# Kernel tuning notes

Measured on AMD Instinct MI355X. Metric: run time of the kernel, lower is better.

Reference implementation:

```python
import jax, jax.numpy as jnp
import numpy as np

N_NODES = 100000
N_EDGES = 3200000
F_IN = 512
HIDDEN = 16
N_CLASS = 10


def gcn_conv(x, edge_index, W, b):
    """PyG-style GCNConv: sym-normalized aggregation with self-loops.
    out = D^{-1/2} (A + I) D^{-1/2} X W + b
    """
    n = x.shape[0]
    loop = jnp.arange(n, dtype=edge_index.dtype)
    src = jnp.concatenate([edge_index[0], loop])  # [E+N]
    dst = jnp.concatenate([edge_index[1], loop])  # [E+N]
    # degree of target nodes (includes self-loops, so deg >= 1)
    deg = jax.ops.segment_sum(jnp.ones_like(src, dtype=x.dtype), dst, num_segments=n)
    dinv = jax.lax.rsqrt(deg)  # safe: deg >= 1
    norm = dinv[src] * dinv[dst]  # [E+N]
    h = x @ W  # [N, out] — transform before gather (cheaper when out < in)
    msg = h[src] * norm[:, None]  # gather + scale
    out = jax.ops.segment_sum(msg, dst, num_segments=n)  # scatter-add
    return out + b


def setup_inputs() -> dict:
    key = jax.random.key(0)
    k1, k2, k3, k4, k5, k6 = jax.random.split(key, 6)
    x = jax.random.normal(k1, (N_NODES, F_IN), dtype=jnp.float32)
    edge_index = jax.random.randint(k2, (2, N_EDGES), 0, N_NODES, dtype=jnp.int64)
    s1 = 1.0 / np.sqrt(F_IN)
    s2 = 1.0 / np.sqrt(HIDDEN)
    W1 = jax.random.uniform(k3, (F_IN, HIDDEN), jnp.float32, -s1, s1)
    b1 = jax.random.uniform(k4, (HIDDEN,), jnp.float32, -s1, s1)
    W2 = jax.random.uniform(k5, (HIDDEN, N_CLASS), jnp.float32, -s2, s2)
    b2 = jax.random.uniform(k6, (N_CLASS,), jnp.float32, -s2, s2)
    return {"x": x, "edge_index": edge_index, "W1": W1, "b1": b1, "W2": W2, "b2": b2}


def reference(x, edge_index, W1, b1, W2, b2):
    h = gcn_conv(x, edge_index, W1, b1)
    h = jax.nn.relu(h)
    # Dropout(p=0.5) is identity in eval/inference mode
    out = gcn_conv(h, edge_index, W2, b2)
    return out
```

## Files before the change

### kernel.cpp

```cpp
#include <hip/hip_runtime.h>

#define N_NODES 100000
#define N_EDGES 3200000
#define F_IN    512
#define HIDDEN  16
#define N_CLASS 10

#define NBUCK   196
#define BSH     9
#define EPB     4096
#define NPART   ((N_EDGES + EPB - 1) / EPB)
#define PCAP    18432

__device__ __forceinline__ int load_idx(const void* ei, int is32, long long pos) {
    return is32 ? ((const int*)ei)[pos] : (int)((const long long*)ei)[pos];
}

__global__ void k_init(const unsigned* __restrict__ ei, int* __restrict__ bsize,
                       int* __restrict__ det) {
    int t = threadIdx.x;
    if (t < NBUCK) bsize[t] = 0;
    if (t == 0) det[0] = 0;
    __syncthreads();
    unsigned odd = 0;
    for (int i = t; i < 4096; i += 256) odd |= ei[2 * i + 1];
    if (odd) atomicOr(&det[0], 1);
}

__global__ __launch_bounds__(256) void k_bhist(const void* __restrict__ ei,
                                               const int* __restrict__ det,
                                               int* __restrict__ bsize) {
    __shared__ int hist[NBUCK];
    int t = threadIdx.x;
    long long e0 = (long long)blockIdx.x * EPB;
    long long e1 = e0 + EPB; if (e1 > N_EDGES) e1 = N_EDGES;
    int is32 = det[0];
    if (t < NBUCK) hist[t] = 0;
    __syncthreads();
    for (long long e = e0 + t; e < e1; e += 256) {
        int d = load_idx(ei, is32, N_EDGES + e);
        atomicAdd(&hist[d >> BSH], 1);
    }
    __syncthreads();
    if (t < NBUCK && hist[t]) atomicAdd(&bsize[t], hist[t]);
}

__global__ void k_bucketscan(const int* __restrict__ bsize, int* __restrict__ bbase,
                             int* __restrict__ bcur) {
    __shared__ int s[256];
    int t = threadIdx.x;
    int v = (t < NBUCK) ? bsize[t] : 0;
    s[t] = v;
    __syncthreads();
    for (int off = 1; off < 256; off <<= 1) {
        int u = (t >= off) ? s[t - off] : 0;
        __syncthreads();
        s[t] += u;
        __syncthreads();
    }
    if (t < NBUCK) { int ex = s[t] - v; bbase[t] = ex; bcur[t] = ex; }
}

__global__ __launch_bounds__(256) void k_part(const void* __restrict__ ei,
                                              const int* __restrict__ det,
                                              int* __restrict__ bcur,
                                              unsigned* __restrict__ buf) {
    __shared__ int hist[NBUCK];
    __shared__ int base[NBUCK];
    __shared__ int lcur[NBUCK];
    int t = threadIdx.x;
    long long e0 = (long long)blockIdx.x * EPB;
    long long e1 = e0 + EPB; if (e1 > N_EDGES) e1 = N_EDGES;
    int is32 = det[0];
    if (t < NBUCK) { hist[t] = 0; lcur[t] = 0; }
    __syncthreads();
    for (long long e = e0 + t; e < e1; e += 256) {
        int d = load_idx(ei, is32, N_EDGES + e);
        atomicAdd(&hist[d >> BSH], 1);
    }
    __syncthreads();
    if (t < NBUCK) base[t] = hist[t] ? atomicAdd(&bcur[t], hist[t]) : 0;
    __syncthreads();
    for (long long e = e0 + t; e < e1; e += 256) {
        int s = load_idx(ei, is32, e);
        int d = load_idx(ei, is32, (long long)N_EDGES + e);
        int b = d >> BSH;
        int off = atomicAdd(&lcur[b], 1);
        buf[base[b] + off] = ((unsigned)s << BSH) | (unsigned)(d & 511);
    }
}

__global__ __launch_bounds__(256) void k_degscan(const unsigned* __restrict__ buf,
                                                 const int* __restrict__ bbase,
                                                 const int* __restrict__ bsize,
                                                 int* __restrict__ rowptr,
                                                 float* __restrict__ dinv) {
    __shared__ int s[512];
    int t = threadIdx.x;
    int b = blockIdx.x;
    s[t] = 0; s[t + 256] = 0;
    __syncthreads();
    int j0 = bbase[b], j1 = j0 + bsize[b];
    for (int j = j0 + t; j < j1; j += 256)
        atomicAdd(&s[buf[j] & 511], 1);
    __syncthreads();
    int o0 = s[t], o1 = s[t + 256];
    for (int off = 1; off < 512; off <<= 1) {
        int v0 = (t >= off) ? s[t - off] : 0;
        int v1 = s[t + 256 - off];
        __syncthreads();
        s[t] += v0; s[t + 256] += v1;
        __syncthreads();
    }
    int nb0 = b << BSH;
    int base = bbase[b];
    int n0 = nb0 + t, n1 = nb0 + t + 256;
    if (n0 < N_NODES) { rowptr[n0] = base + s[t] - o0;       dinv[n0] = rsqrtf((float)(o0 + 1)); }
    if (n1 < N_NODES) { rowptr[n1] = base + s[t + 256] - o1; dinv[n1] = rsqrtf((float)(o1 + 1)); }
    if (b == NBUCK - 1 && t == 0) rowptr[N_NODES] = N_EDGES;
}

__global__ __launch_bounds__(256) void k_place3(const unsigned* __restrict__ buf,
                                                const int* __restrict__ bbase,
                                                const int* __restrict__ bsize,
                                                const int* __restrict__ rowptr,
                                                int* __restrict__ csr) {
    __shared__ int lptr[512];
    __shared__ int outb[PCAP];
    int t = threadIdx.x;
    int b = blockIdx.x;
    int jb = bbase[b];
    int sz = bsize[b];
    int nb0 = b << BSH;
    int csrbase = rowptr[nb0];
    for (int i = t; i < 512; i += 256) {
        int n = nb0 + i;
        lptr[i] = (n < N_NODES) ? rowptr[n] - csrbase : sz;
    }
    __syncthreads();
    for (int j = t; j < sz; j += 256) {
        unsigned p = buf[jb + j];
        int pos = atomicAdd(&lptr[p & 511], 1);
        int s = (int)(p >> BSH);
        if (pos < PCAP) outb[pos] = s;
        else            csr[csrbase + pos] = s;
    }
    __syncthreads();
    int lim = sz < PCAP ? sz : PCAP;
    for (int j = t; j < lim; j += 256) csr[csrbase + j] = outb[j];
}

__global__ __launch_bounds__(128) void k_gemv1(const float* __restrict__ x,
                                               const float* __restrict__ W1,
                                               const float* __restrict__ dinv,
                                               float* __restrict__ hs) {
    int n = blockIdx.x * 128 + threadIdx.x;
    if (n >= N_NODES) return;
    const float4* xr = (const float4*)(x + (size_t)n * F_IN);
    float acc[16];
#pragma unroll
    for (int k = 0; k < 16; ++k) acc[k] = 0.f;
#pragma unroll 1
    for (int ch = 0; ch < F_IN / 64; ++ch) {
        float4 v[16];
#pragma unroll
        for (int i = 0; i < 16; ++i) v[i] = xr[ch * 16 + i];
#pragma unroll
        for (int i = 0; i < 16; ++i) {
            const float* wp = &W1[(ch * 64 + i * 4) * HIDDEN];
#pragma unroll
            for (int k = 0; k < 16; ++k)
                acc[k] += v[i].x * wp[k]      + v[i].y * wp[16 + k]
                        + v[i].z * wp[32 + k] + v[i].w * wp[48 + k];
        }
    }
    float di = dinv[n];
    float4* o = (float4*)&hs[(size_t)n * HIDDEN];
    o[0] = make_float4(acc[0] * di,  acc[1] * di,  acc[2] * di,  acc[3] * di);
    o[1] = make_float4(acc[4] * di,  acc[5] * di,  acc[6] * di,  acc[7] * di);
    o[2] = make_float4(acc[8] * di,  acc[9] * di,  acc[10] * di, acc[11] * di);
    o[3] = make_float4(acc[12] * di, acc[13] * di, acc[14] * di, acc[15] * di);
}

__global__ __launch_bounds__(256) void k_agg1(const int* __restrict__ rowptr,
                                              const int* __restrict__ csr,
                                              const float* __restrict__ hs,
                                              const float* __restrict__ dinv,
                                              const float* __restrict__ b1,
                                              const float* __restrict__ W2,
                                              float* __restrict__ ts) {
    __shared__ float sh[16][17];
    int t  = threadIdx.x;
    int ln = t >> 4;
    int k  = t & 15;
    int n  = blockIdx.x * 16 + ln;
    bool valid = n < N_NODES;
    int r0 = valid ? rowptr[n] : 0;
    int r1 = valid ? rowptr[n + 1] : 0;
    float acc = valid ? hs[(size_t)n * HIDDEN + k] : 0.f;
    int j = r0;
    for (; j + 4 <= r1; j += 4) {
        int s0 = csr[j], s1 = csr[j + 1], s2 = csr[j + 2], s3 = csr[j + 3];
        float v0 = hs[(size_t)s0 * HIDDEN + k];
        float v1 = hs[(size_t)s1 * HIDDEN + k];
        float v2 = hs[(size_t)s2 * HIDDEN + k];
        float v3 = hs[(size_t)s3 * HIDDEN + k];
        acc += (v0 + v1) + (v2 + v3);
    }
    for (; j < r1; ++j) acc += hs[(size_t)csr[j] * HIDDEN + k];
    float di = valid ? dinv[n] : 0.f;
    float h = di * acc + b1[k];
    sh[ln][k] = h > 0.f ? h : 0.f;
    __syncthreads();
    int c = (k < N_CLASS) ? k : 0;
    float o = 0.f;
#pragma unroll
    for (int kk = 0; kk < HIDDEN; ++kk) o += sh[ln][kk] * W2[kk * N_CLASS + c];
    if (valid) ts[(size_t)n * 16 + k] = (k < N_CLASS) ? o * di : 0.f;
}

__global__ __launch_bounds__(256) void k_agg2(const int* __restrict__ rowptr,
                                              const int* __restrict__ csr,
                                              const float* __restrict__ ts,
                                              const float* __restrict__ dinv,
                                              const float* __restrict__ b2,
                                              float* __restrict__ out) {
    int t  = threadIdx.x;
    int ln = t >> 4;
    int c  = t & 15;
    int n  = blockIdx.x * 16 + ln;
    if (n >= N_NODES) return;
    int r0 = rowptr[n], r1 = rowptr[n + 1];
    float acc = ts[(size_t)n * 16 + c];
    int j = r0;
    for (; j + 4 <= r1; j += 4) {
        int s0 = csr[j], s1 = csr[j + 1], s2 = csr[j + 2], s3 = csr[j + 3];
        float v0 = ts[(size_t)s0 * 16 + c];
        float v1 = ts[(size_t)s1 * 16 + c];
        float v2 = ts[(size_t)s2 * 16 + c];
        float v3 = ts[(size_t)s3 * 16 + c];
        acc += (v0 + v1) + (v2 + v3);
    }
    for (; j < r1; ++j) acc += ts[(size_t)csr[j] * 16 + c];
    if (c < N_CLASS) out[(size_t)n * N_CLASS + c] = dinv[n] * acc + b2[c];
}

extern "C" void kernel_launch(void* const* d_in, const int* in_sizes, int n_in,
                              void* d_out, int out_size, void* d_ws, size_t ws_size,
                              hipStream_t stream) {
    const float* x  = (const float*)d_in[0];
    const void*  ei = d_in[1];
    const float* W1 = (const float*)d_in[2];
    const float* b1 = (const float*)d_in[3];
    const float* W2 = (const float*)d_in[4];
    const float* b2 = (const float*)d_in[5];
    float* out = (float*)d_out;
    float* ws  = (float*)d_ws;

    float* dinv   = ws;
    int*   rowptr = (int*)(ws + 100096);
    int*   bsize  = (int*)(ws + 200512);
    int*   bbase  = (int*)(ws + 200768);
    int*   bcur   = (int*)(ws + 201024);
    int*   det    = (int*)(ws + 201280);
    int*   csr    = (int*)(ws + 201344);
    float* hs     = ws + 3401344;
    float* ts     = ws + 5001344;
    unsigned* buf = (unsigned*)(ws + 3401344);

    k_init      <<<1, 256, 0, stream>>>((const unsigned*)ei, bsize, det);
    k_bhist     <<<NPART, 256, 0, stream>>>(ei, det, bsize);
    k_bucketscan<<<1, 256, 0, stream>>>(bsize, bbase, bcur);
    k_part      <<<NPART, 256, 0, stream>>>(ei, det, bcur, buf);
    k_degscan   <<<NBUCK, 256, 0, stream>>>(buf, bbase, bsize, rowptr, dinv);
    k_place3    <<<NBUCK, 256, 0, stream>>>(buf, bbase, bsize, rowptr, csr);

    k_gemv1<<<(N_NODES + 127) / 128, 128, 0, stream>>>(x, W1, dinv, hs);

    k_agg1<<<(N_NODES + 15) / 16, 256, 0, stream>>>(rowptr, csr, hs, dinv, b1, W2, ts);
    k_agg2<<<(N_NODES + 15) / 16, 256, 0, stream>>>(rowptr, csr, ts, dinv, b2, out);
}
```

Before: 606.1 us.

## Split GEMV K-dimension across four waves and unroll aggregation gathers by eight

The first-layer GEMV now assigns four threads per node, each covering a quarter of the 512 input features with register double-buffered loads, then reduces the partial sums through shared memory. This raises the number of threads in flight for the 205 MB read of x and shortens each thread's serial chain, at the cost of a shared-memory reduction and a barrier. Both aggregation kernels also gain an 8-way unrolled gather loop so more independent loads are outstanding per thread.

```diff
diff --git a/kernel.cpp b/kernel.cpp
--- a/kernel.cpp
+++ b/kernel.cpp
@@ -150,36 +150,63 @@
     for (int j = t; j < lim; j += 256) csr[csrbase + j] = outb[j];
 }
 
-__global__ __launch_bounds__(128) void k_gemv1(const float* __restrict__ x,
+__global__ __launch_bounds__(256) void k_gemv1(const float* __restrict__ x,
                                                const float* __restrict__ W1,
                                                const float* __restrict__ dinv,
                                                float* __restrict__ hs) {
-    int n = blockIdx.x * 128 + threadIdx.x;
-    if (n >= N_NODES) return;
-    const float4* xr = (const float4*)(x + (size_t)n * F_IN);
+    __shared__ float red[3][64][17];
+    int t = threadIdx.x;
+    int r = t & 63;
+    int seg = t >> 6;
+    int n = blockIdx.x * 64 + r;
+    bool valid = n < N_NODES;
+    const float4* xr = (const float4*)(x + (valid ? (size_t)n * F_IN : 0) + seg * 128);
     float acc[16];
 #pragma unroll
     for (int k = 0; k < 16; ++k) acc[k] = 0.f;
+    float4 cur0 = xr[0], cur1 = xr[1], cur2 = xr[2], cur3 = xr[3];
 #pragma unroll 1
-    for (int ch = 0; ch < F_IN / 64; ++ch) {
-        float4 v[16];
-#pragma unroll
-        for (int i = 0; i < 16; ++i) v[i] = xr[ch * 16 + i];
-#pragma unroll
-        for (int i = 0; i < 16; ++i) {
-            const float* wp = &W1[(ch * 64 + i * 4) * HIDDEN];
-#pragma unroll
-            for (int k = 0; k < 16; ++k)
-                acc[k] += v[i].x * wp[k]      + v[i].y * wp[16 + k]
-                        + v[i].z * wp[32 + k] + v[i].w * wp[48 + k];
+    for (int ch = 0; ch < 8; ++ch) {
+        float4 nx0, nx1, nx2, nx3;
+        if (ch < 7) {
+            nx0 = xr[(ch + 1) * 4 + 0]; nx1 = xr[(ch + 1) * 4 + 1];
+            nx2 = xr[(ch + 1) * 4 + 2]; nx3 = xr[(ch + 1) * 4 + 3];
         }
-    }
-    float di = dinv[n];
-    float4* o = (float4*)&hs[(size_t)n * HIDDEN];
-    o[0] = make_float4(acc[0] * di,  acc[1] * di,  acc[2] * di,  acc[3] * di);
-    o[1] = make_float4(acc[4] * di,  acc[5] * di,  acc[6] * di,  acc[7] * di);
-    o[2] = make_float4(acc[8] * di,  acc[9] * di,  acc[10] * di, acc[11] * di);
-    o[3] = make_float4(acc[12] * di, acc[13] * di, acc[14] * di, acc[15] * di);
+        const float* wp = W1 + (seg * 128 + ch * 16) * HIDDEN;
+#pragma unroll
+        for (int k = 0; k < 16; ++k)
+            acc[k] += cur0.x * wp[0 * 16 + k] + cur0.y * wp[1 * 16 + k]
+                    + cur0.z * wp[2 * 16 + k] + cur0.w * wp[3 * 16 + k];
+#pragma unroll
+        for (int k = 0; k < 16; ++k)
+            acc[k] += cur1.x * wp[4 * 16 + k] + cur1.y * wp[5 * 16 + k]
+                    + cur1.z * wp[6 * 16 + k] + cur1.w * wp[7 * 16 + k];
+#pragma unroll
+        for (int k = 0; k < 16; ++k)
+            acc[k] += cur2.x * wp[8 * 16 + k] + cur2.y * wp[9 * 16 + k]
+                    + cur2.z * wp[10 * 16 + k] + cur2.w * wp[11 * 16 + k];
+#pragma unroll
+        for (int k = 0; k < 16; ++k)
+            acc[k] += cur3.x * wp[12 * 16 + k] + cur3.y * wp[13 * 16 + k]
+                    + cur3.z * wp[14 * 16 + k] + cur3.w * wp[15 * 16 + k];
+        if (ch < 7) { cur0 = nx0; cur1 = nx1; cur2 = nx2; cur3 = nx3; }
+    }
+    if (seg) {
+#pragma unroll
+        for (int k = 0; k < 16; ++k) red[seg - 1][r][k] = acc[k];
+    }
+    __syncthreads();
+    if (seg == 0 && valid) {
+#pragma unroll
+        for (int k = 0; k < 16; ++k)
+            acc[k] += red[0][r][k] + red[1][r][k] + red[2][r][k];
+        float di = dinv[n];
+        float4* o = (float4*)&hs[(size_t)n * HIDDEN];
+        o[0] = make_float4(acc[0] * di,  acc[1] * di,  acc[2] * di,  acc[3] * di);
+        o[1] = make_float4(acc[4] * di,  acc[5] * di,  acc[6] * di,  acc[7] * di);
+        o[2] = make_float4(acc[8] * di,  acc[9] * di,  acc[10] * di, acc[11] * di);
+        o[3] = make_float4(acc[12] * di, acc[13] * di, acc[14] * di, acc[15] * di);
+    }
 }
 
 __global__ __launch_bounds__(256) void k_agg1(const int* __restrict__ rowptr,
@@ -199,6 +226,19 @@
     int r1 = valid ? rowptr[n + 1] : 0;
     float acc = valid ? hs[(size_t)n * HIDDEN + k] : 0.f;
     int j = r0;
+    for (; j + 8 <= r1; j += 8) {
+        int s0 = csr[j],     s1 = csr[j + 1], s2 = csr[j + 2], s3 = csr[j + 3];
+        int s4 = csr[j + 4], s5 = csr[j + 5], s6 = csr[j + 6], s7 = csr[j + 7];
+        float v0 = hs[(size_t)s0 * HIDDEN + k];
+        float v1 = hs[(size_t)s1 * HIDDEN + k];
+        float v2 = hs[(size_t)s2 * HIDDEN + k];
+        float v3 = hs[(size_t)s3 * HIDDEN + k];
+        float v4 = hs[(size_t)s4 * HIDDEN + k];
+        float v5 = hs[(size_t)s5 * HIDDEN + k];
+        float v6 = hs[(size_t)s6 * HIDDEN + k];
+        float v7 = hs[(size_t)s7 * HIDDEN + k];
+        acc += ((v0 + v1) + (v2 + v3)) + ((v4 + v5) + (v6 + v7));
+    }
     for (; j + 4 <= r1; j += 4) {
         int s0 = csr[j], s1 = csr[j + 1], s2 = csr[j + 2], s3 = csr[j + 3];
         float v0 = hs[(size_t)s0 * HIDDEN + k];
@@ -233,6 +273,19 @@
     int r0 = rowptr[n], r1 = rowptr[n + 1];
     float acc = ts[(size_t)n * 16 + c];
     int j = r0;
+    for (; j + 8 <= r1; j += 8) {
+        int s0 = csr[j],     s1 = csr[j + 1], s2 = csr[j + 2], s3 = csr[j + 3];
+        int s4 = csr[j + 4], s5 = csr[j + 5], s6 = csr[j + 6], s7 = csr[j + 7];
+        float v0 = ts[(size_t)s0 * 16 + c];
+        float v1 = ts[(size_t)s1 * 16 + c];
+        float v2 = ts[(size_t)s2 * 16 + c];
+        float v3 = ts[(size_t)s3 * 16 + c];
+        float v4 = ts[(size_t)s4 * 16 + c];
+        float v5 = ts[(size_t)s5 * 16 + c];
+        float v6 = ts[(size_t)s6 * 16 + c];
+        float v7 = ts[(size_t)s7 * 16 + c];
+        acc += ((v0 + v1) + (v2 + v3)) + ((v4 + v5) + (v6 + v7));
+    }
     for (; j + 4 <= r1; j += 4) {
         int s0 = csr[j], s1 = csr[j + 1], s2 = csr[j + 2], s3 = csr[j + 3];
         float v0 = ts[(size_t)s0 * 16 + c];
@@ -275,7 +328,7 @@
     k_degscan   <<<NBUCK, 256, 0, stream>>>(buf, bbase, bsize, rowptr, dinv);
     k_place3    <<<NBUCK, 256, 0, stream>>>(buf, bbase, bsize, rowptr, csr);
 
-    k_gemv1<<<(N_NODES + 127) / 128, 128, 0, stream>>>(x, W1, dinv, hs);
+    k_gemv1<<<(N_NODES + 63) / 64, 256, 0, stream>>>(x, W1, dinv, hs);
 
     k_agg1<<<(N_NODES + 15) / 16, 256, 0, stream>>>(rowptr, csr, hs, dinv, b1, W2, ts);
     k_agg2<<<(N_NODES + 15) / 16, 256, 0, stream>>>(rowptr, csr, ts, dinv, b2, out);
```

Result: faster. 585.6 us (-3.4%).
